# Kernel optimization log

Hardware: AMD Instinct MI355X
Metric: run time of the kernel (lower is better)

Reference implementation:

```python
import jax, jax.numpy as jnp
import numpy as np

N_MLPS = 256
N_BLOCKS = 8
TCODE = 13
IN_F = 3
HID = 128
OUT_F = 1
B = 256
NPTS = 2048
K = 256  # 8-bit codebook
OMEGA = 30.0

# per-layer (fan_in, fan_out) for weight reconstruction
LAYER_SHAPES = [(IN_F + TCODE, HID), (HID, HID), (HID, HID), (HID, OUT_F)]


def setup_inputs() -> dict:
    key = jax.random.key(0)
    ks = jax.random.split(key, 20)
    inp = {
        "x": jax.random.uniform(ks[0], (B, NPTS, IN_F), jnp.float32, -1.0, 1.0),
        "mlp_idx": jax.random.randint(ks[1], (B,), 0, N_MLPS, jnp.int32),
        "block_idx": jax.random.randint(ks[2], (B,), 0, N_BLOCKS, jnp.int32),
        "latent_table": jax.random.normal(ks[3], (N_MLPS, N_BLOCKS, TCODE), jnp.float32),
    }
    for l, (fi, fo) in enumerate(LAYER_SHAPES):
        bound = 1.0 / np.sqrt(fi)
        inp[f"centroids_l{l}"] = jax.random.uniform(ks[4 + 3 * l], (K,), jnp.float32, -bound, bound)
        inp[f"labels_l{l}"] = jax.random.randint(ks[5 + 3 * l], (N_MLPS * fi * fo,), 0, K, jnp.int32)
        inp[f"bias_l{l}"] = jax.random.uniform(ks[6 + 3 * l], (N_MLPS, 1, fo), jnp.float32, -bound, bound)
    return inp


def _layer(h, idx, centroids, labels, bias, fi, fo, apply_sin):
    # codebook dequant: weight.view(-1)[:] = centroids[labels]
    weight = centroids[labels].reshape(N_MLPS, fi, fo)
    # indexed bmm: torch.bmm(x, weight[indices]) + bias[indices]
    out = jnp.einsum("bni,bio->bno", h, weight[idx]) + bias[idx]
    return jnp.sin(OMEGA * out) if apply_sin else out


def reference(x, mlp_idx, block_idx, latent_table,
              centroids_l0, labels_l0, bias_l0,
              centroids_l1, labels_l1, bias_l1,
              centroids_l2, labels_l2, bias_l2,
              centroids_l3, labels_l3, bias_l3):
    # gather per-sample latent code and concat with coords
    z = latent_table[mlp_idx, block_idx]                      # [B, TCODE]
    h = jnp.concatenate(
        [x, jnp.broadcast_to(z[:, None, :], (x.shape[0], x.shape[1], TCODE))], axis=-1)
    cs = [centroids_l0, centroids_l1, centroids_l2, centroids_l3]
    ls = [labels_l0, labels_l1, labels_l2, labels_l3]
    bs = [bias_l0, bias_l1, bias_l2, bias_l3]
    for l, (fi, fo) in enumerate(LAYER_SHAPES):
        h = _layer(h, mlp_idx, cs[l], ls[l], bs[l], fi, fo, apply_sin=(l < len(LAYER_SHAPES) - 1))
    return h
```

## Files before the change

kernel.cpp:

```cpp
#include <hip/hip_runtime.h>


typedef unsigned int u32;
typedef unsigned short u16;
typedef __bf16 v8bf  __attribute__((ext_vector_type(8)));
typedef __bf16 v2bf  __attribute__((ext_vector_type(2)));
typedef float  v16f  __attribute__((ext_vector_type(16)));
typedef float  v2f   __attribute__((ext_vector_type(2)));
typedef u32    v4u   __attribute__((ext_vector_type(4)));
typedef u32    v2u   __attribute__((ext_vector_type(2)));

#define MFMA(a, b, c) __builtin_amdgcn_mfma_f32_32x32x16_bf16(a, b, c, 0, 0, 0)

#define HSTRIDE 136
#define OMEGA_S 4.774648292756860f

__device__ __forceinline__ float sinrev(float rev) {
    return __builtin_amdgcn_sinf(__builtin_amdgcn_fractf(rev));
}

__device__ __forceinline__ u32 pack2(float c) {
    __bf16 b0 = (__bf16)c;
    float  f0 = (float)b0;
    __bf16 b1 = (__bf16)(c - f0);
    return (u32)__builtin_bit_cast(u16, b0) |
           ((u32)__builtin_bit_cast(u16, b1) << 16);
}

__device__ __forceinline__ void pk2(float s0, float s1, u32& lo, u32& hi) {
    v2f s; s[0] = s0; s[1] = s1;
    v2bf l = __builtin_convertvector(s, v2bf);
    u32 lov = __builtin_bit_cast(u32, l);
    v2f lf;
    lf[0] = __builtin_bit_cast(float, lov << 16);
    lf[1] = __builtin_bit_cast(float, lov & 0xffff0000u);
    v2f r = s - lf;
    v2bf h = __builtin_convertvector(r, v2bf);
    lo = lov;
    hi = __builtin_bit_cast(u32, h);
}

__device__ __forceinline__ u32 pklo(float s0, float s1) {
    v2f s; s[0] = s0; s[1] = s1;
    v2bf l = __builtin_convertvector(s, v2bf);
    return __builtin_bit_cast(u32, l);
}

#define PLO(a, b) __builtin_amdgcn_perm((a), (b), 0x05040100u)
#define PHI(a, b) __builtin_amdgcn_perm((a), (b), 0x07060302u)

__global__ __launch_bounds__(512)
void ecnr_dequant(const float* __restrict__ cent0, const int* __restrict__ lab0,
                  const float* __restrict__ cent1, const int* __restrict__ lab1,
                  const float* __restrict__ cent2, const int* __restrict__ lab2,
                  const float* __restrict__ cent3, const int* __restrict__ lab3,
                  const float* __restrict__ bias0, const float* __restrict__ bias1,
                  const float* __restrict__ bias2,
                  u16* __restrict__ wpl1, u16* __restrict__ wpl2,
                  u16* __restrict__ w0pl, u16* __restrict__ w3pl,
                  float* __restrict__ biasc)
{
    __shared__ u32 cpk[512];
    const int t = threadIdx.x;

    if (blockIdx.x < 512) {
        const int m = blockIdx.x >> 1, L = blockIdx.x & 1;
        if (t < 256) cpk[t] = pack2((L ? cent2 : cent1)[t] * OMEGA_S);
        __syncthreads();
        const int* lab = (L ? lab2 : lab1) + (size_t)m * 16384;
        u16* base = (L ? wpl2 : wpl1) + (size_t)m * 32768;
        #pragma unroll
        for (int i = 0; i < 4; ++i) {
            const int id = i * 512 + t;
            const int n = id & 127, c = id >> 7;
            u32 g[8];
            #pragma unroll
            for (int j = 0; j < 8; ++j) g[j] = cpk[lab[(8 * c + j) * 128 + n]];
            v4u lo, hi;
            #pragma unroll
            for (int r = 0; r < 4; ++r) {
                lo[r] = PLO(g[2 * r + 1], g[2 * r]);
                hi[r] = PHI(g[2 * r + 1], g[2 * r]);
            }
            *(v4u*)(base + c * 1024 + n * 8)         = lo;
            *(v4u*)(base + 16384 + c * 1024 + n * 8) = hi;
        }
    } else {
        const int m = blockIdx.x - 512;
        if (t < 256) cpk[t] = pack2(cent0[t] * OMEGA_S);
        else         cpk[t] = pack2(cent3[t - 256]);
        __syncthreads();
        if (t < 256) {
            const int n = t & 127, c = t >> 7;
            const int* lab = lab0 + (size_t)m * 2048;
            u32 g[8];
            #pragma unroll
            for (int j = 0; j < 8; ++j) g[j] = cpk[lab[(8 * c + j) * 128 + n]];
            v4u lo, hi;
            #pragma unroll
            for (int r = 0; r < 4; ++r) {
                lo[r] = PLO(g[2 * r + 1], g[2 * r]);
                hi[r] = PHI(g[2 * r + 1], g[2 * r]);
            }
            u16* b0 = w0pl + (size_t)m * 4096;
            *(v4u*)(b0 + c * 1024 + n * 8)        = lo;
            *(v4u*)(b0 + 2048 + c * 1024 + n * 8) = hi;
        } else if (t < 384) {
            const int kk = t - 256;
            const u32 u = cpk[256 + lab3[(size_t)m * 128 + kk]];
            w3pl[(size_t)m * 256 + kk]       = (u16)u;
            w3pl[(size_t)m * 256 + 128 + kk] = (u16)(u >> 16);
        }
        if (t < 384) {
            const int li = t >> 7, kk = t & 127;
            const float* bsrc = (li == 0) ? bias0 : (li == 1) ? bias1 : bias2;
            biasc[(size_t)m * 384 + t] = bsrc[m * 128 + kk] * OMEGA_S;
        }
    }
}


#define EPI_FULL(ACC, LOP, HIP)                                   \
    do {                                                          \
        _Pragma("unroll")                                         \
        for (int gg = 0; gg < 4; ++gg) {                          \
            const float s0 = sinrev((ACC)[4 * gg + 0]);           \
            const float s1 = sinrev((ACC)[4 * gg + 1]);           \
            const float s2 = sinrev((ACC)[4 * gg + 2]);           \
            const float s3 = sinrev((ACC)[4 * gg + 3]);           \
            u32 l0, h0, l1, h1;                                   \
            pk2(s0, s1, l0, h0);                                  \
            pk2(s2, s3, l1, h1);                                  \
            v2u lov, hiv;                                         \
            lov[0] = l0; lov[1] = l1;                             \
            hiv[0] = h0; hiv[1] = h1;                             \
            *(v2u*)((LOP) + 8 * gg) = lov;                        \
            *(v2u*)((HIP) + 8 * gg) = hiv;                        \
        }                                                         \
    } while (0)

#define EPI_LO(ACC, LOP)                                          \
    do {                                                          \
        _Pragma("unroll")                                         \
        for (int gg = 0; gg < 4; ++gg) {                          \
            const float s0 = sinrev((ACC)[4 * gg + 0]);           \
            const float s1 = sinrev((ACC)[4 * gg + 1]);           \
            const float s2 = sinrev((ACC)[4 * gg + 2]);           \
            const float s3 = sinrev((ACC)[4 * gg + 3]);           \
            v2u lov;                                              \
            lov[0] = pklo(s0, s1);                                \
            lov[1] = pklo(s2, s3);                                \
            *(v2u*)((LOP) + 8 * gg) = lov;                        \
        }                                                         \
    } while (0)

__global__ __launch_bounds__(256, 4)
void ecnr_fwd(const float* __restrict__ x,
              const int*   __restrict__ mlp_idx,
              const int*   __restrict__ block_idx,
              const float* __restrict__ latent,
              const float* __restrict__ bias3,
              const u16* __restrict__ wpl1, const u16* __restrict__ wpl2,
              const u16* __restrict__ w0pl, const u16* __restrict__ w3pl,
              const float* __restrict__ biasc,
              float* __restrict__ out)
{
    __shared__ __attribute__((aligned(16))) u16   Hlo[64 * HSTRIDE];
    __shared__ __attribute__((aligned(16))) u16   Hhi[64 * HSTRIDE];
    __shared__ __attribute__((aligned(16))) float biasS[2 * 128];
    __shared__ __attribute__((aligned(16))) float red[2 * 128];

    const int g    = blockIdx.x;
    const int b    = ((g >> 8) << 3) | (g & 7);
    const int p0   = ((g >> 3) & 31) * 64;
    const int m    = mlp_idx[b];

    const int t  = threadIdx.x;
    const int l  = t & 63, nt = t >> 6;
    const int q  = l >> 5, ln = l & 31;
    const int nn   = nt * 32 + ln;
    const int bidx = nt * 32 + 4 * q;

    const float* bc = biasc + (size_t)m * 384;
    if (t < 128) {
        biasS[t]       = bc[128 + t];
        biasS[128 + t] = bc[256 + t];
    }
    const float* xpA = x + (size_t)(b * 2048 + p0 + ln) * 3;
    const float xA0 = xpA[0], xA1 = xpA[1], xA2 = xpA[2];
    const float xB0 = xpA[96], xB1 = xpA[97], xB2 = xpA[98];
    const u16* w0p = w0pl + (size_t)m * 4096 + q * 1024 + nn * 8;
    const v4u w0lo = *(const v4u*)(w0p);
    const v4u w0hi = *(const v4u*)(w0p + 2048);
    float4 b0f[4];
    #pragma unroll
    for (int gg = 0; gg < 4; ++gg)
        b0f[gg] = *(const float4*)(bc + bidx + 8 * gg);
    const float* zp = latent + ((size_t)m * 8 + block_idx[b]) * 13;
    float zr[8];
    #pragma unroll
    for (int j = 0; j < 8; ++j) zr[j] = zp[q * 5 + j];

    u16* lopA = Hlo + ln * HSTRIDE + nt * 32 + 4 * q;
    u16* hipA = Hhi + ln * HSTRIDE + nt * 32 + 4 * q;
    u16* lopB = lopA + 32 * HSTRIDE;
    u16* hipB = hipA + 32 * HSTRIDE;

    {
        float finA[8], finB[8];
        if (q == 0) {
            finA[0] = xA0; finA[1] = xA1; finA[2] = xA2;
            finB[0] = xB0; finB[1] = xB1; finB[2] = xB2;
            #pragma unroll
            for (int j = 0; j < 5; ++j) { finA[3 + j] = zr[j]; finB[3 + j] = zr[j]; }
        } else {
            #pragma unroll
            for (int j = 0; j < 8; ++j) { finA[j] = zr[j]; finB[j] = zr[j]; }
        }
        v4u ilA, ihA, ilB, ihB;
        #pragma unroll
        for (int r = 0; r < 4; ++r) {
            u32 plo, phi;
            pk2(finA[2 * r], finA[2 * r + 1], plo, phi);
            ilA[r] = plo; ihA[r] = phi;
            pk2(finB[2 * r], finB[2 * r + 1], plo, phi);
            ilB[r] = plo; ihB[r] = phi;
        }
        const v8bf inloA = __builtin_bit_cast(v8bf, ilA);
        const v8bf inhiA = __builtin_bit_cast(v8bf, ihA);
        const v8bf inloB = __builtin_bit_cast(v8bf, ilB);
        const v8bf inhiB = __builtin_bit_cast(v8bf, ihB);
        const v8bf wl = __builtin_bit_cast(v8bf, w0lo);
        const v8bf wh = __builtin_bit_cast(v8bf, w0hi);
        v16f accA, accB;
        #pragma unroll
        for (int gg = 0; gg < 4; ++gg) {
            accA[4 * gg] = b0f[gg].x; accA[4 * gg + 1] = b0f[gg].y;
            accA[4 * gg + 2] = b0f[gg].z; accA[4 * gg + 3] = b0f[gg].w;
            accB[4 * gg] = b0f[gg].x; accB[4 * gg + 1] = b0f[gg].y;
            accB[4 * gg + 2] = b0f[gg].z; accB[4 * gg + 3] = b0f[gg].w;
        }
        __builtin_amdgcn_s_setprio(1);
        accA = MFMA(wl, inloA, accA); accB = MFMA(wl, inloB, accB);
        accA = MFMA(wl, inhiA, accA); accB = MFMA(wl, inhiB, accB);
        accA = MFMA(wh, inloA, accA); accB = MFMA(wh, inloB, accB);
        __builtin_amdgcn_s_setprio(0);
        EPI_FULL(accA, lopA, hipA);
        EPI_FULL(accB, lopB, hipB);
    }
    __syncthreads();

    const u16* HLA = Hlo + ln * HSTRIDE + q * 8;
    const u16* HHA = Hhi + ln * HSTRIDE + q * 8;
    const u16* HLB = HLA + 32 * HSTRIDE;
    const u16* HHB = HHA + 32 * HSTRIDE;
    #pragma unroll 1
    for (int L = 0; L < 2; ++L) {
        const u16* Wb = (L ? wpl2 : wpl1) + (size_t)m * 32768 + q * 1024 + nn * 8;
        v16f accA, accB;
        #pragma unroll
        for (int gg = 0; gg < 4; ++gg) {
            const float4 bv = *(const float4*)&biasS[L * 128 + bidx + 8 * gg];
            accA[4 * gg] = bv.x; accA[4 * gg + 1] = bv.y;
            accA[4 * gg + 2] = bv.z; accA[4 * gg + 3] = bv.w;
            accB[4 * gg] = bv.x; accB[4 * gg + 1] = bv.y;
            accB[4 * gg + 2] = bv.z; accB[4 * gg + 3] = bv.w;
        }
        v4u wl8[8];
        #pragma unroll
        for (int kc = 0; kc < 8; ++kc)
            wl8[kc] = *(const v4u*)(Wb + kc * 2048);
        #pragma unroll
        for (int kc = 0; kc < 8; ++kc) {
            const v4u whv = *(const v4u*)(Wb + kc * 2048 + 16384);
            const v8bf hloA = *(const v8bf*)(HLA + kc * 16);
            const v8bf hhiA = *(const v8bf*)(HHA + kc * 16);
            const v8bf hloB = *(const v8bf*)(HLB + kc * 16);
            const v8bf hhiB = *(const v8bf*)(HHB + kc * 16);
            const v8bf wlv = __builtin_bit_cast(v8bf, wl8[kc]);
            const v8bf whb = __builtin_bit_cast(v8bf, whv);
            __builtin_amdgcn_s_setprio(1);
            accA = MFMA(wlv, hloA, accA); accB = MFMA(wlv, hloB, accB);
            accA = MFMA(wlv, hhiA, accA); accB = MFMA(wlv, hhiB, accB);
            accA = MFMA(whb, hloA, accA); accB = MFMA(whb, hloB, accB);
            __builtin_amdgcn_s_setprio(0);
        }
        __syncthreads();
        if (L == 0) {
            EPI_FULL(accA, lopA, hipA);
            EPI_FULL(accB, lopB, hipB);
        } else {
            EPI_LO(accA, lopA);
            EPI_LO(accB, lopB);
        }
        __syncthreads();
    }

    {
        const u16* w3b = w3pl + (size_t)m * 256 + nt * 32 + q * 8;
        const u16* h3A = Hlo + ln * HSTRIDE + nt * 32 + q * 8;
        const u16* h3B = h3A + 32 * HSTRIDE;
        v16f aA, aB;
        #pragma unroll
        for (int r = 0; r < 16; ++r) { aA[r] = 0.0f; aB[r] = 0.0f; }
        #pragma unroll
        for (int kc = 0; kc < 2; ++kc) {
            const v8bf wl = *(const v8bf*)(w3b + kc * 16);
            const v8bf wh = *(const v8bf*)(w3b + 128 + kc * 16);
            const v8bf hA = *(const v8bf*)(h3A + kc * 16);
            const v8bf hB = *(const v8bf*)(h3B + kc * 16);
            __builtin_amdgcn_s_setprio(1);
            aA = MFMA(wl, hA, aA); aB = MFMA(wl, hB, aB);
            aA = MFMA(wh, hA, aA); aB = MFMA(wh, hB, aB);
            __builtin_amdgcn_s_setprio(0);
        }
        if (q == 0) {
            red[nt * 32 + ln]       = aA[0];
            red[128 + nt * 32 + ln] = aB[0];
        }
    }
    __syncthreads();

    if (t < 64) {
        const int rp = (t >> 5) * 128, rl = t & 31;
        const float o = bias3[m]
            + red[rp + rl] + red[rp + 32 + rl]
            + red[rp + 64 + rl] + red[rp + 96 + rl];
        out[(size_t)b * 2048 + p0 + t] = o;
    }
}

extern "C" void kernel_launch(void* const* d_in, const int* in_sizes, int n_in,
                              void* d_out, int out_size, void* d_ws, size_t ws_size,
                              hipStream_t stream) {
    (void)in_sizes; (void)n_in; (void)out_size; (void)ws_size;
    u16*   wpl1  = (u16*)d_ws;
    u16*   wpl2  = wpl1 + (size_t)256 * 32768;
    u16*   w0pl  = wpl2 + (size_t)256 * 32768;
    u16*   w3pl  = w0pl + (size_t)256 * 4096;
    float* biasc = (float*)(w3pl + (size_t)256 * 256);

    ecnr_dequant<<<768, 512, 0, stream>>>(
        (const float*)d_in[4],  (const int*)d_in[5],
        (const float*)d_in[7],  (const int*)d_in[8],
        (const float*)d_in[10], (const int*)d_in[11],
        (const float*)d_in[13], (const int*)d_in[14],
        (const float*)d_in[6],  (const float*)d_in[9], (const float*)d_in[12],
        wpl1, wpl2, w0pl, w3pl, biasc);

    ecnr_fwd<<<8192, 256, 0, stream>>>(
        (const float*)d_in[0], (const int*)d_in[1], (const int*)d_in[2],
        (const float*)d_in[3],
        (const float*)d_in[15],
        wpl1, wpl2, w0pl, w3pl, biasc,
        (float*)d_out);
}
```

Baseline: 222.6 us.

## Swizzle activation LDS layout, drop padding and bias smem to raise occupancy

Replaces the padded activation tile (stride 136) with an unpadded stride-128 layout that uses an XOR swizzle on 16-byte chunks to avoid LDS bank conflicts. Bias values are read straight from global memory instead of being staged in shared memory, and the reduction buffer now reuses the Hhi array. The smaller LDS footprint lets launch bounds ask for 5 blocks per CU instead of 4, trading possible register pressure and extra address arithmetic for higher occupancy.

```diff
diff --git a/kernel.cpp b/kernel.cpp
--- a/kernel.cpp
+++ b/kernel.cpp
@@ -12,7 +12,7 @@
 
 #define MFMA(a, b, c) __builtin_amdgcn_mfma_f32_32x32x16_bf16(a, b, c, 0, 0, 0)
 
-#define HSTRIDE 136
+#define HSTRIDE 128
 #define OMEGA_S 4.774648292756860f
 
 __device__ __forceinline__ float sinrev(float rev) {
@@ -120,10 +120,11 @@
 }
 
 
-#define EPI_FULL(ACC, LOP, HIP)                                   \
+#define EPI_FULL(ACC, ROWLO, ROWHI)                               \
     do {                                                          \
         _Pragma("unroll")                                         \
         for (int gg = 0; gg < 4; ++gg) {                          \
+            const int wo = (((4 * nt + gg) ^ key) << 3) + 4 * q;  \
             const float s0 = sinrev((ACC)[4 * gg + 0]);           \
             const float s1 = sinrev((ACC)[4 * gg + 1]);           \
             const float s2 = sinrev((ACC)[4 * gg + 2]);           \
@@ -134,15 +135,16 @@
             v2u lov, hiv;                                         \
             lov[0] = l0; lov[1] = l1;                             \
             hiv[0] = h0; hiv[1] = h1;                             \
-            *(v2u*)((LOP) + 8 * gg) = lov;                        \
-            *(v2u*)((HIP) + 8 * gg) = hiv;                        \
+            *(v2u*)((ROWLO) + wo) = lov;                          \
+            *(v2u*)((ROWHI) + wo) = hiv;                          \
         }                                                         \
     } while (0)
 
-#define EPI_LO(ACC, LOP)                                          \
+#define EPI_LO(ACC, ROWLO)                                        \
     do {                                                          \
         _Pragma("unroll")                                         \
         for (int gg = 0; gg < 4; ++gg) {                          \
+            const int wo = (((4 * nt + gg) ^ key) << 3) + 4 * q;  \
             const float s0 = sinrev((ACC)[4 * gg + 0]);           \
             const float s1 = sinrev((ACC)[4 * gg + 1]);           \
             const float s2 = sinrev((ACC)[4 * gg + 2]);           \
@@ -150,11 +152,11 @@
             v2u lov;                                              \
             lov[0] = pklo(s0, s1);                                \
             lov[1] = pklo(s2, s3);                                \
-            *(v2u*)((LOP) + 8 * gg) = lov;                        \
+            *(v2u*)((ROWLO) + wo) = lov;                          \
         }                                                         \
     } while (0)
 
-__global__ __launch_bounds__(256, 4)
+__global__ __launch_bounds__(256, 5)
 void ecnr_fwd(const float* __restrict__ x,
               const int*   __restrict__ mlp_idx,
               const int*   __restrict__ block_idx,
@@ -165,10 +167,9 @@
               const float* __restrict__ biasc,
               float* __restrict__ out)
 {
-    __shared__ __attribute__((aligned(16))) u16   Hlo[64 * HSTRIDE];
-    __shared__ __attribute__((aligned(16))) u16   Hhi[64 * HSTRIDE];
-    __shared__ __attribute__((aligned(16))) float biasS[2 * 128];
-    __shared__ __attribute__((aligned(16))) float red[2 * 128];
+    __shared__ __attribute__((aligned(16))) u16 Hlo[64 * HSTRIDE];
+    __shared__ __attribute__((aligned(16))) u16 Hhi[64 * HSTRIDE];
+    float* red = (float*)Hhi;
 
     const int g    = blockIdx.x;
     const int b    = ((g >> 8) << 3) | (g & 7);
@@ -180,12 +181,9 @@
     const int q  = l >> 5, ln = l & 31;
     const int nn   = nt * 32 + ln;
     const int bidx = nt * 32 + 4 * q;
+    const int key  = ln & 15;
 
     const float* bc = biasc + (size_t)m * 384;
-    if (t < 128) {
-        biasS[t]       = bc[128 + t];
-        biasS[128 + t] = bc[256 + t];
-    }
     const float* xpA = x + (size_t)(b * 2048 + p0 + ln) * 3;
     const float xA0 = xpA[0], xA1 = xpA[1], xA2 = xpA[2];
     const float xB0 = xpA[96], xB1 = xpA[97], xB2 = xpA[98];
@@ -201,10 +199,10 @@
     #pragma unroll
     for (int j = 0; j < 8; ++j) zr[j] = zp[q * 5 + j];
 
-    u16* lopA = Hlo + ln * HSTRIDE + nt * 32 + 4 * q;
-    u16* hipA = Hhi + ln * HSTRIDE + nt * 32 + 4 * q;
-    u16* lopB = lopA + 32 * HSTRIDE;
-    u16* hipB = hipA + 32 * HSTRIDE;
+    u16* rowloA = Hlo + ln * HSTRIDE;
+    u16* rowhiA = Hhi + ln * HSTRIDE;
+    u16* rowloB = rowloA + 32 * HSTRIDE;
+    u16* rowhiB = rowhiA + 32 * HSTRIDE;
 
     {
         float finA[8], finB[8];
@@ -245,22 +243,19 @@
         accA = MFMA(wl, inhiA, accA); accB = MFMA(wl, inhiB, accB);
         accA = MFMA(wh, inloA, accA); accB = MFMA(wh, inloB, accB);
         __builtin_amdgcn_s_setprio(0);
-        EPI_FULL(accA, lopA, hipA);
-        EPI_FULL(accB, lopB, hipB);
+        EPI_FULL(accA, rowloA, rowhiA);
+        EPI_FULL(accB, rowloB, rowhiB);
     }
     __syncthreads();
 
-    const u16* HLA = Hlo + ln * HSTRIDE + q * 8;
-    const u16* HHA = Hhi + ln * HSTRIDE + q * 8;
-    const u16* HLB = HLA + 32 * HSTRIDE;
-    const u16* HHB = HHA + 32 * HSTRIDE;
     #pragma unroll 1
     for (int L = 0; L < 2; ++L) {
         const u16* Wb = (L ? wpl2 : wpl1) + (size_t)m * 32768 + q * 1024 + nn * 8;
+        const float* bL = bc + 128 + (L << 7) + bidx;
         v16f accA, accB;
         #pragma unroll
         for (int gg = 0; gg < 4; ++gg) {
-            const float4 bv = *(const float4*)&biasS[L * 128 + bidx + 8 * gg];
+            const float4 bv = *(const float4*)(bL + 8 * gg);
             accA[4 * gg] = bv.x; accA[4 * gg + 1] = bv.y;
             accA[4 * gg + 2] = bv.z; accA[4 * gg + 3] = bv.w;
             accB[4 * gg] = bv.x; accB[4 * gg + 1] = bv.y;
@@ -273,10 +268,11 @@
         #pragma unroll
         for (int kc = 0; kc < 8; ++kc) {
             const v4u whv = *(const v4u*)(Wb + kc * 2048 + 16384);
-            const v8bf hloA = *(const v8bf*)(HLA + kc * 16);
-            const v8bf hhiA = *(const v8bf*)(HHA + kc * 16);
-            const v8bf hloB = *(const v8bf*)(HLB + kc * 16);
-            const v8bf hhiB = *(const v8bf*)(HHB + kc * 16);
+            const int ro = (((2 * kc + q) ^ key) << 3);
+            const v8bf hloA = *(const v8bf*)(rowloA + ro);
+            const v8bf hhiA = *(const v8bf*)(rowhiA + ro);
+            const v8bf hloB = *(const v8bf*)(rowloB + ro);
+            const v8bf hhiB = *(const v8bf*)(rowhiB + ro);
             const v8bf wlv = __builtin_bit_cast(v8bf, wl8[kc]);
             const v8bf whb = __builtin_bit_cast(v8bf, whv);
             __builtin_amdgcn_s_setprio(1);
@@ -287,28 +283,27 @@
         }
         __syncthreads();
         if (L == 0) {
-            EPI_FULL(accA, lopA, hipA);
-            EPI_FULL(accB, lopB, hipB);
+            EPI_FULL(accA, rowloA, rowhiA);
+            EPI_FULL(accB, rowloB, rowhiB);
         } else {
-            EPI_LO(accA, lopA);
-            EPI_LO(accB, lopB);
+            EPI_LO(accA, rowloA);
+            EPI_LO(accB, rowloB);
         }
         __syncthreads();
     }
 
     {
         const u16* w3b = w3pl + (size_t)m * 256 + nt * 32 + q * 8;
-        const u16* h3A = Hlo + ln * HSTRIDE + nt * 32 + q * 8;
-        const u16* h3B = h3A + 32 * HSTRIDE;
         v16f aA, aB;
         #pragma unroll
         for (int r = 0; r < 16; ++r) { aA[r] = 0.0f; aB[r] = 0.0f; }
         #pragma unroll
         for (int kc = 0; kc < 2; ++kc) {
+            const int o3 = (((4 * nt + 2 * kc + q) ^ key) << 3);
             const v8bf wl = *(const v8bf*)(w3b + kc * 16);
             const v8bf wh = *(const v8bf*)(w3b + 128 + kc * 16);
-            const v8bf hA = *(const v8bf*)(h3A + kc * 16);
-            const v8bf hB = *(const v8bf*)(h3B + kc * 16);
+            const v8bf hA = *(const v8bf*)(rowloA + o3);
+            const v8bf hB = *(const v8bf*)(rowloB + o3);
             __builtin_amdgcn_s_setprio(1);
             aA = MFMA(wl, hA, aA); aB = MFMA(wl, hB, aB);
             aA = MFMA(wh, hA, aA); aB = MFMA(wh, hB, aB);
```

Result: slower. 288.8 us (+29.7%).
